# Kernel optimization log

Measured on AMD Instinct MI355X. Metric: run time of the kernel, lower is better.

## Reference

```python
import jax, jax.numpy as jnp
import numpy as np

HID_DIM = 1024
B, S = 8, 2048
SCALE = float(np.sqrt(HID_DIM))
NEG = -1e10


def setup_inputs() -> dict:
    key = jax.random.key(0)
    ks = jax.random.split(key, 13)
    d = HID_DIM
    std = 1.0 / np.sqrt(d)
    return {
        "query": jax.random.normal(ks[0], (B, S, d), jnp.float32),
        "key_": jax.random.normal(ks[1], (B, S, d), jnp.float32),
        "value": jax.random.normal(ks[2], (B, S, d), jnp.float32),
        "mask": jax.random.randint(ks[3], (B, S), 0, 2, jnp.int32),
        "Wq": jax.random.uniform(ks[4], (d, d), jnp.float32, -std, std),
        "bq": jax.random.uniform(ks[5], (d,), jnp.float32, -std, std),
        "Wk": jax.random.uniform(ks[6], (d, d), jnp.float32, -std, std),
        "bk": jax.random.uniform(ks[7], (d,), jnp.float32, -std, std),
        "Wv": jax.random.uniform(ks[8], (d, d), jnp.float32, -std, std),
        "bv": jax.random.uniform(ks[9], (d,), jnp.float32, -std, std),
        "Wfc": jax.random.uniform(ks[10], (d, d), jnp.float32, -std, std),
        "bfc": jax.random.uniform(ks[11], (d,), jnp.float32, -std, std),
    }


def reference(query, key_, value, mask, Wq, bq, Wk, bk, Wv, bv, Wfc, bfc):
    # Linear projections (torch Linear: x @ W.T + b)
    Q = jnp.einsum("bsd,ed->bse", query, Wq) + bq
    K = jnp.einsum("bsd,ed->bse", key_, Wk) + bk
    V = jnp.einsum("bsd,ed->bse", value, Wv) + bv
    # Scaled dot-product energy: [B, S, S]
    energy = jnp.einsum("bqd,bkd->bqk", Q, K) / SCALE
    # Faithful to source: mask broadcast over last dim masks QUERY rows
    energy = jnp.where(mask[:, :, None] == 0, NEG, energy)
    attention = jax.nn.softmax(energy, axis=-1)  # dropout=0 (eval)
    x = jnp.einsum("bqk,bkd->bqd", attention, V)
    out = jnp.einsum("bsd,ed->bse", x, Wfc) + bfc
    return out
```

## Files before the change

### kernel.cpp

```cpp
#include <hip/hip_runtime.h>
#include <hip/hip_bf16.h>


#define DEVINL __device__ __forceinline__

typedef __bf16 bf16x8 __attribute__((ext_vector_type(8)));
typedef float f32x4 __attribute__((ext_vector_type(4)));

static constexpr int Bb = 8;
static constexpr int S = 2048;
static constexpr int D = 1024;

DEVINL unsigned short f32_to_bf16(float f) {
  unsigned u = __float_as_uint(f);
  u = (u + 0x7FFFu + ((u >> 16) & 1u)) >> 16;
  return (unsigned short)u;
}
DEVINL float bflo(unsigned u) { return __uint_as_float(u << 16); }
DEVINL float bfhi(unsigned u) { return __uint_as_float(u & 0xFFFF0000u); }

DEVINL void gload16(const unsigned short* g, char* l) {
  __builtin_amdgcn_global_load_lds((__attribute__((address_space(1))) void*)g,
                                   (__attribute__((address_space(3))) void*)l,
                                   16, 0, 0);
}
DEVINL void gload16u(const unsigned short* g, unsigned short* l) {
  gload16(g, (char*)l);
}

#define BAR() __builtin_amdgcn_s_barrier()
#define LGK0() asm volatile("s_waitcnt lgkmcnt(0)" ::: "memory")

#define PH_OPEN() \
  BAR();          \
  LGK0();         \
  __builtin_amdgcn_s_setprio(1)
#define PH_CLOSE()               \
  __builtin_amdgcn_s_setprio(0); \
  BAR()

#define MFMA_QUAD(A_, B_, MO, NO)                                              \
  {                                                                            \
    _Pragma("unroll") for (int mi_ = 0; mi_ < 4; mi_++) {                      \
      _Pragma("unroll") for (int nj_ = 0; nj_ < 2; nj_++) {                    \
        acc[(MO) + mi_][(NO) + nj_] = __builtin_amdgcn_mfma_f32_16x16x32_bf16( \
            A_[mi_][0], B_[nj_][0], acc[(MO) + mi_][(NO) + nj_], 0, 0, 0);     \
        acc[(MO) + mi_][(NO) + nj_] = __builtin_amdgcn_mfma_f32_16x16x32_bf16( \
            A_[mi_][1], B_[nj_][1], acc[(MO) + mi_][(NO) + nj_], 0, 0, 0);     \
      }                                                                        \
    }                                                                          \
  }

__global__ __launch_bounds__(256) void conv_f32_bf16(const float* __restrict__ in,
                                                     unsigned short* __restrict__ out,
                                                     int n8) {
  int i = blockIdx.x * 256 + threadIdx.x;
  int stride = gridDim.x * 256;
  for (; i < n8; i += stride) {
    const float4* p = (const float4*)in + (size_t)i * 2;
    float4 a = p[0], b = p[1];
    uint4 o;
    o.x = (unsigned)f32_to_bf16(a.x) | ((unsigned)f32_to_bf16(a.y) << 16);
    o.y = (unsigned)f32_to_bf16(a.z) | ((unsigned)f32_to_bf16(a.w) << 16);
    o.z = (unsigned)f32_to_bf16(b.x) | ((unsigned)f32_to_bf16(b.y) << 16);
    o.w = (unsigned)f32_to_bf16(b.z) | ((unsigned)f32_to_bf16(b.w) << 16);
    ((uint4*)out)[i] = o;
  }
}

__global__ __launch_bounds__(256) void conv_k_wvec(const float* __restrict__ in,
                                                   const float* __restrict__ g32,
                                                   unsigned short* __restrict__ xkB,
                                                   float* __restrict__ w32) {
  const int row = blockIdx.x * 4 + (threadIdx.x >> 6);
  const int lane = threadIdx.x & 63;
  const float* src = in + (size_t)row * 1024 + lane * 16;
  unsigned short* dst = xkB + (size_t)row * 1024 + lane * 16;
  float s = 0.f;
  uint4 o[2];
  unsigned* po = (unsigned*)o;
#pragma unroll
  for (int c = 0; c < 4; c++) {
    float4 v = *(const float4*)(src + c * 4);
    float4 g = *(const float4*)(g32 + lane * 16 + c * 4);
    unsigned lo = (unsigned)f32_to_bf16(v.x) | ((unsigned)f32_to_bf16(v.y) << 16);
    unsigned hi = (unsigned)f32_to_bf16(v.z) | ((unsigned)f32_to_bf16(v.w) << 16);
    po[c * 2] = lo;
    po[c * 2 + 1] = hi;
    s += bflo(lo) * g.x + bfhi(lo) * g.y + bflo(hi) * g.z + bfhi(hi) * g.w;
  }
  *(uint4*)dst = o[0];
  *(uint4*)(dst + 8) = o[1];
#pragma unroll
  for (int off = 32; off >= 1; off >>= 1) s += __shfl_xor(s, off);
  if (lane == 0) w32[row] = s;
}

__global__ __launch_bounds__(256) void tconv(const float* __restrict__ in,
                                             unsigned short* __restrict__ out,
                                             int R, int C) {
  __shared__ unsigned short t[64][72];
  const int c0 = blockIdx.x * 64, r0 = blockIdx.y * 64, b = blockIdx.z;
  in += (size_t)b * R * C;
  out += (size_t)b * R * C;
  const int tr = threadIdx.x >> 4;
  const int tc = threadIdx.x & 15;
#pragma unroll
  for (int i = 0; i < 4; i++) {
    int row = tr + i * 16;
    float4 v = *(const float4*)(in + (size_t)(r0 + row) * C + c0 + tc * 4);
    t[tc * 4 + 0][row] = f32_to_bf16(v.x);
    t[tc * 4 + 1][row] = f32_to_bf16(v.y);
    t[tc * 4 + 2][row] = f32_to_bf16(v.z);
    t[tc * 4 + 3][row] = f32_to_bf16(v.w);
  }
  __syncthreads();
  const int c = threadIdx.x >> 2, rs = (threadIdx.x & 3) * 16;
  unsigned short tmp[16];
#pragma unroll
  for (int j = 0; j < 16; j++) tmp[j] = t[c][rs + j];
  *(uint4*)(out + (size_t)(c0 + c) * R + r0 + rs) = *(const uint4*)&tmp[0];
  *(uint4*)(out + (size_t)(c0 + c) * R + r0 + rs + 8) = *(const uint4*)&tmp[8];
}

__global__ __launch_bounds__(256) void cvec_kernel(const float* __restrict__ Wfc,
                                                   const float* __restrict__ bv,
                                                   const float* __restrict__ bfc,
                                                   float* __restrict__ cv) {
  const int f = blockIdx.x;
  const float* row = Wfc + (size_t)f * 1024;
  float s = 0.f;
  for (int e = threadIdx.x; e < 1024; e += 256) s += row[e] * bv[e];
#pragma unroll
  for (int off = 32; off >= 1; off >>= 1) s += __shfl_xor(s, off);
  __shared__ float red[4];
  const int wave = threadIdx.x >> 6, lane = threadIdx.x & 63;
  if (lane == 0) red[wave] = s;
  __syncthreads();
  if (threadIdx.x == 0) cv[f] = red[0] + red[1] + red[2] + red[3] + bfc[f];
}

__global__ __launch_bounds__(256) void gvec_kernel(const unsigned short* __restrict__ WkT,
                                                   const float* __restrict__ bq,
                                                   float* __restrict__ g32) {
  const int e = blockIdx.x;
  const unsigned short* row = WkT + (size_t)e * 1024;
  const int j0 = threadIdx.x * 4;
  uint2 v = *(const uint2*)(row + j0);
  float4 b4 = *(const float4*)(bq + j0);
  float s = bflo(v.x) * b4.x + bfhi(v.x) * b4.y + bflo(v.y) * b4.z + bfhi(v.y) * b4.w;
#pragma unroll
  for (int off = 32; off >= 1; off >>= 1) s += __shfl_xor(s, off);
  __shared__ float red[4];
  const int wave = threadIdx.x >> 6, lane = threadIdx.x & 63;
  if (lane == 0) red[wave] = s;
  __syncthreads();
  if (threadIdx.x == 0) g32[e] = (red[0] + red[1] + red[2] + red[3]) * (1.0f / 32.0f);
}

__global__ __launch_bounds__(256) void mask_scan(const int* __restrict__ msk,
                                                 int* __restrict__ qidx,
                                                 int* __restrict__ midx,
                                                 int* __restrict__ cnts) {
  __shared__ int offs[257];
  const int b = blockIdx.x;
  const int* mrow = msk + b * 2048;
  const int base = threadIdx.x * 8;
  int m[8], c = 0;
#pragma unroll
  for (int i = 0; i < 8; i++) {
    m[i] = mrow[base + i];
    c += m[i];
  }
  offs[threadIdx.x + 1] = c;
  __syncthreads();
  if (threadIdx.x == 0) {
    offs[0] = 0;
    for (int j = 1; j <= 256; j++) offs[j] += offs[j - 1];
    int tot = offs[256];
    cnts[b] = tot;
    cnts[8 + b] = (tot + 127) & ~127;
    cnts[16 + b] = (tot + 255) & ~255;
    cnts[24 + b] = 2048 - tot;
  }
  __syncthreads();
  int u = offs[threadIdx.x];
#pragma unroll
  for (int i = 0; i < 8; i++) {
    int idx = base + i;
    if (m[i])
      qidx[b * 2048 + (u++)] = idx;
    else
      midx[b * 2048 + (idx - u)] = idx;
  }
}

__global__ __launch_bounds__(128) void compact_q(const float* __restrict__ q,
                                                 const int* __restrict__ qidx,
                                                 const int* __restrict__ cnts,
                                                 unsigned short* __restrict__ xqC) {
  const int r = blockIdx.x;
  const int b = r >> 11, i = r & 2047;
  if (i >= cnts[16 + b]) return;
  unsigned short* dst = xqC + ((size_t)b * 2048 + i) * 1024;
  if (i < cnts[b]) {
    const float* src = q + ((size_t)b * 2048 + qidx[b * 2048 + i]) * 1024 + threadIdx.x * 8;
    float4 a = *(const float4*)src;
    float4 c = *(const float4*)(src + 4);
    uint4 o;
    o.x = (unsigned)f32_to_bf16(a.x) | ((unsigned)f32_to_bf16(a.y) << 16);
    o.y = (unsigned)f32_to_bf16(a.z) | ((unsigned)f32_to_bf16(a.w) << 16);
    o.z = (unsigned)f32_to_bf16(c.x) | ((unsigned)f32_to_bf16(c.y) << 16);
    o.w = (unsigned)f32_to_bf16(c.z) | ((unsigned)f32_to_bf16(c.w) << 16);
    ((uint4*)dst)[threadIdx.x] = o;
  } else {
    ((uint4*)dst)[threadIdx.x] = make_uint4(0, 0, 0, 0);
  }
}

__global__ __launch_bounds__(64) void colmean_kernel(const unsigned short* __restrict__ vpT,
                                                     const float* __restrict__ cv,
                                                     float* __restrict__ cm) {
  const int f = blockIdx.x, b = blockIdx.y;
  const unsigned short* base = vpT + (size_t)f * 16384 + b * 2048 + threadIdx.x * 32;
  float s = 0.f;
#pragma unroll
  for (int c = 0; c < 4; c++) {
    uint4 v = ((const uint4*)base)[c];
    unsigned u[4] = {v.x, v.y, v.z, v.w};
#pragma unroll
    for (int i = 0; i < 4; i++) s += bflo(u[i]) + bfhi(u[i]);
  }
#pragma unroll
  for (int off = 32; off >= 1; off >>= 1) s += __shfl_xor(s, off);
  if (threadIdx.x == 0) cm[b * 1024 + f] = s * (1.0f / 2048.0f) + cv[f];
}

__global__ __launch_bounds__(128) void fill_masked(const int* __restrict__ midx,
                                                   const int* __restrict__ cnts,
                                                   const float* __restrict__ cm,
                                                   float* __restrict__ out) {
  const int r = blockIdx.x;
  const int b = r >> 11, j = r & 2047;
  if (j >= cnts[24 + b]) return;
  const int qr = midx[b * 2048 + j];
  float* dst = out + ((size_t)b * 2048 + qr) * 1024 + threadIdx.x * 8;
  const float* src = cm + b * 1024 + threadIdx.x * 8;
  *(float4*)dst = *(const float4*)src;
  *(float4*)(dst + 4) = *(const float4*)(src + 4);
}

__global__ __launch_bounds__(256) void rowinv_kernel(const float* __restrict__ partialT,
                                                     float* __restrict__ rowinv) {
  const int r = blockIdx.x * 256 + threadIdx.x;
  float s = 0.f;
#pragma unroll
  for (int c = 0; c < 32; c++) s += partialT[(size_t)c * 16384 + r];
  rowinv[r] = 1.0f / s;
}

__global__ __launch_bounds__(256) void gemm128(const unsigned short* __restrict__ A,
                                               const unsigned short* __restrict__ Bt,
                                               unsigned short* __restrict__ C,
                                               int M, int N, int K,
                                               long long bsA, long long bsB, long long bsC) {
  const int tid = threadIdx.x;
  const int wave = tid >> 6;
  const int lane = tid & 63;
  const int wr = wave >> 1, wc = wave & 1;
  const int m0 = blockIdx.y * 128, n0 = blockIdx.x * 128;
  A += (size_t)blockIdx.z * bsA;
  Bt += (size_t)blockIdx.z * bsB;
  C += (size_t)blockIdx.z * bsC;

  __shared__ unsigned short lds[2][2][128 * 32];

  const int srow = wave * 16 + (lane >> 2);
  const int scol = (lane & 3) * 8;
  const unsigned short* gA = A + (size_t)(m0 + srow) * K + scol;
  const unsigned short* gB = Bt + (size_t)(n0 + srow) * K + scol;

  f32x4 acc[4][4];
#pragma unroll
  for (int i = 0; i < 4; i++)
#pragma unroll
    for (int j = 0; j < 4; j++) acc[i][j] = (f32x4){0.f, 0.f, 0.f, 0.f};

  const int nk = K >> 5;
  auto stage = [&](int buf, int kt) {
    const unsigned short* a0 = gA + (size_t)kt * 32;
    const unsigned short* b0 = gB + (size_t)kt * 32;
    unsigned short* la = &lds[buf][0][wave * 512];
    unsigned short* lb = &lds[buf][1][wave * 512];
    gload16u(a0, la);
    gload16u(a0 + (size_t)64 * K, la + 2048);
    gload16u(b0, lb);
    gload16u(b0 + (size_t)64 * K, lb + 2048);
  };

  stage(0, 0);
  asm volatile("s_waitcnt vmcnt(0)" ::: "memory");
  __syncthreads();

  const int fm = lane & 15;
  const int fk = (lane >> 4) * 8;

  int cur = 0;
  for (int t = 0; t < nk; ++t) {
    if (t + 1 < nk) stage(cur ^ 1, t + 1);
    bf16x8 af[4], bfr[4];
#pragma unroll
    for (int i = 0; i < 4; i++)
      af[i] = *(const bf16x8*)&lds[cur][0][(wr * 64 + i * 16 + fm) * 32 + fk];
#pragma unroll
    for (int j = 0; j < 4; j++)
      bfr[j] = *(const bf16x8*)&lds[cur][1][(wc * 64 + j * 16 + fm) * 32 + fk];
#pragma unroll
    for (int i = 0; i < 4; i++)
#pragma unroll
      for (int j = 0; j < 4; j++)
        acc[i][j] = __builtin_amdgcn_mfma_f32_16x16x32_bf16(af[i], bfr[j], acc[i][j], 0, 0, 0);
    asm volatile("s_waitcnt vmcnt(0)" ::: "memory");
    __syncthreads();
    cur ^= 1;
  }

  const int en = n0 + wc * 64 + fm;
  const int em = m0 + wr * 64 + ((lane >> 4) << 2);
#pragma unroll
  for (int j = 0; j < 4; j++)
#pragma unroll
    for (int i = 0; i < 4; i++)
#pragma unroll
      for (int r = 0; r < 4; r++)
        C[(size_t)(em + i * 16 + r) * N + en + j * 16] = f32_to_bf16(acc[i][j][r]);
}

template <int OUTMODE>
__global__ __launch_bounds__(256, 3) void gemm128c(
    const unsigned short* __restrict__ A, const unsigned short* __restrict__ Bt,
    const float* __restrict__ aux,
    const float* __restrict__ bias,
    const int* __restrict__ cnts, const int* __restrict__ qidx,
    float* __restrict__ partialT, void* __restrict__ Cv,
    int N, int K, int lda, int ldb,
    long long bsA, long long bsB, long long bsC, float scale) {
  __shared__ unsigned short lds[2][2][128 * 32];
  char* smem = (char*)&lds[0][0][0];
  const int tid = threadIdx.x;
  const int wave = tid >> 6, lane = tid & 63;
  const int wm = wave >> 1, wn = wave & 1;

  const int gx = gridDim.x, gy = gridDim.y;
  const int nwg = gx * gy * (int)gridDim.z;
  const int wg = blockIdx.x + gx * (blockIdx.y + gy * blockIdx.z);
  const int swz = (wg & 7) * (nwg >> 3) + (wg >> 3);
  const int bx = swz % gx;
  const int rem = swz / gx;
  const int by = rem % gy;
  const int bz = rem / gy;

  const int m0 = by * 128, n0 = bx * 128;
  if (OUTMODE == 3) {
    if (n0 >= cnts[8 + bz]) return;
  } else {
    if (m0 >= cnts[8 + bz]) return;
  }
  A += (size_t)bz * bsA;
  Bt += (size_t)bz * bsB;

  const int srow = wave * 16 + (lane >> 2);
  const int scol = (lane & 3) * 8;
  const unsigned short* gA = A + (size_t)(m0 + srow) * lda + scol;
  const unsigned short* gB = Bt + (size_t)(n0 + srow) * ldb + scol;

  f32x4 acc[4][4];
#pragma unroll
  for (int i = 0; i < 4; i++)
#pragma unroll
    for (int j = 0; j < 4; j++) acc[i][j] = (f32x4){0.f, 0.f, 0.f, 0.f};

  const int nk = K >> 5;
  auto stage = [&](int buf, int kt) {
    const unsigned short* a0 = gA + (size_t)kt * 32;
    const unsigned short* b0 = gB + (size_t)kt * 32;
    unsigned short* la = &lds[buf][0][wave * 512];
    unsigned short* lb = &lds[buf][1][wave * 512];
    gload16u(a0, la);
    gload16u(a0 + (size_t)64 * lda, la + 2048);
    gload16u(b0, lb);
    gload16u(b0 + (size_t)64 * ldb, lb + 2048);
  };

  stage(0, 0);
  asm volatile("s_waitcnt vmcnt(0)" ::: "memory");
  __syncthreads();

  const int fm = lane & 15;
  const int fk = (lane >> 4) * 8;

  int cur = 0;
  for (int t = 0; t < nk; ++t) {
    if (t + 1 < nk) stage(cur ^ 1, t + 1);
    bf16x8 af[4], bfr[4];
#pragma unroll
    for (int i = 0; i < 4; i++)
      af[i] = *(const bf16x8*)&lds[cur][0][(wm * 64 + i * 16 + fm) * 32 + fk];
#pragma unroll
    for (int j = 0; j < 4; j++)
      bfr[j] = *(const bf16x8*)&lds[cur][1][(wn * 64 + j * 16 + fm) * 32 + fk];
    __builtin_amdgcn_s_setprio(1);
#pragma unroll
    for (int i = 0; i < 4; i++)
#pragma unroll
      for (int j = 0; j < 4; j++)
        acc[i][j] = __builtin_amdgcn_mfma_f32_16x16x32_bf16(af[i], bfr[j], acc[i][j], 0, 0, 0);
    __builtin_amdgcn_s_setprio(0);
    asm volatile("s_waitcnt vmcnt(0)" ::: "memory");
    __syncthreads();
    cur ^= 1;
  }

  const int fr = lane & 15;
  const int fg = lane >> 4;

  if (OUTMODE == 3) {
    const int keyrow0 = m0 + wm * 64 + fg * 4;
    const int colq = wn * 64 + fr;
    float psum[4] = {0.f, 0.f, 0.f, 0.f};
#pragma unroll
    for (int mi = 0; mi < 4; mi++) {
      const float4 w4 = *(const float4*)&aux[bz * 2048 + keyrow0 + mi * 16];
      const int lrow = wm * 64 + fg * 4 + mi * 16;
#pragma unroll
      for (int nj = 0; nj < 4; nj++) {
        float p0 = __expf(fmaf(acc[mi][nj][0], scale, w4.x));
        float p1 = __expf(fmaf(acc[mi][nj][1], scale, w4.y));
        float p2 = __expf(fmaf(acc[mi][nj][2], scale, w4.z));
        float p3 = __expf(fmaf(acc[mi][nj][3], scale, w4.w));
        psum[nj] += (p0 + p1) + (p2 + p3);
        unsigned lo = (unsigned)f32_to_bf16(p0) | ((unsigned)f32_to_bf16(p1) << 16);
        unsigned hi = (unsigned)f32_to_bf16(p2) | ((unsigned)f32_to_bf16(p3) << 16);
        const int c = colq + nj * 16;
        const int byte = c * 256 + ((((lrow >> 3) ^ (c & 7)) << 4) | ((lrow & 4) << 1));
        *(uint2*)(smem + byte) = make_uint2(lo, hi);
      }
    }
#pragma unroll
    for (int nj = 0; nj < 4; nj++) {
      psum[nj] += __shfl_xor(psum[nj], 16);
      psum[nj] += __shfl_xor(psum[nj], 32);
    }
    if (fg == 0) {
#pragma unroll
      for (int nj = 0; nj < 4; nj++)
        partialT[(size_t)(by * 2 + wm) * 16384 + bz * 2048 + n0 + colq + nj * 16] = psum[nj];
    }
    __syncthreads();
    unsigned short* Eb = (unsigned short*)Cv + (size_t)bz * bsC;
    const int qh = wave * 2 + (lane >> 5);
    const int kq = (lane & 31) * 4;
#pragma unroll
    for (int p = 0; p < 16; p++) {
      const int ql = qh + p * 8;
      const int byte = ql * 256 + ((((kq >> 3) ^ (ql & 7)) << 4) | ((kq & 4) << 1));
      uint2 vv = *(const uint2*)(smem + byte);
      *(uint2*)(Eb + (size_t)(n0 + ql) * 2048 + m0 + kq) = vv;
    }
  } else {
    float* C = (float*)Cv + (size_t)bz * bsC;
    const int* qx = qidx + bz * 2048;
    const int cb = cnts[bz];
    const int row0base = m0 + wm * 64 + fg * 4;
    const int colbase = n0 + wn * 64 + fr;
#pragma unroll
    for (int mi = 0; mi < 4; mi++) {
      const int j0 = row0base + mi * 16;
      const float4 ri = *(const float4*)&aux[bz * 2048 + j0];
      int qr[4];
      bool ok[4];
#pragma unroll
      for (int r = 0; r < 4; r++) {
        ok[r] = (j0 + r) < cb;
        qr[r] = ok[r] ? qx[j0 + r] : 0;
      }
#pragma unroll
      for (int nj = 0; nj < 4; nj++) {
        const int col = colbase + nj * 16;
        const float cvv = bias[col];
        if (ok[0]) C[(size_t)qr[0] * N + col] = fmaf(acc[mi][nj][0], ri.x, cvv);
        if (ok[1]) C[(size_t)qr[1] * N + col] = fmaf(acc[mi][nj][1], ri.y, cvv);
        if (ok[2]) C[(size_t)qr[2] * N + col] = fmaf(acc[mi][nj][2], ri.z, cvv);
        if (ok[3]) C[(size_t)qr[3] * N + col] = fmaf(acc[mi][nj][3], ri.w, cvv);
      }
    }
  }
}

template <int OUTMODE, bool HAS_BIAS, int EXITMODE>
__global__ __launch_bounds__(512, 2) void gemm256(
    const unsigned short* __restrict__ A, const unsigned short* __restrict__ Bt,
    const float* __restrict__ bias, const int* __restrict__ cnts,
    const int* __restrict__ qidx, float* __restrict__ partial,
    void* __restrict__ Cv, int M, int N, int K, int lda, int ldb,
    long long bsA, long long bsB, long long bsC, float scale) {
  extern __shared__ char smem[];
  const int tid = threadIdx.x;
  const int wave = tid >> 6, lane = tid & 63;
  const int wr = wave >> 2, wc = wave & 3;

  const int gx = gridDim.x, gy = gridDim.y;
  const int nwg = gx * gy * (int)gridDim.z;
  const int wg = blockIdx.x + gx * (blockIdx.y + gy * blockIdx.z);
  const int swz = (wg & 7) * (nwg >> 3) + (wg >> 3);
  const int bx = swz % gx;
  const int rem = swz / gx;
  const int by = rem % gy;
  const int bz = rem / gy;

  const int m0 = by * 256, n0 = bx * 256;
  if (EXITMODE == 1) {
    if ((n0 & 2047) >= cnts[16 + (n0 >> 11)]) return;
  }
  A += (size_t)bz * bsA;
  Bt += (size_t)bz * bsB;

  const int rl = lane >> 3;
  const int gl = (lane & 7) ^ rl;
  const unsigned short* gA = A + (size_t)(m0 + wave * 8 + rl) * lda + gl * 8;
  const unsigned short* gB = Bt + (size_t)(n0 + wave * 8 + rl) * ldb + gl * 8;

  auto stageA = [&](int db, int t, int h) {
    const unsigned short* g = gA + (size_t)(h * 128) * lda + (size_t)t * 64;
    char* l = smem + db * 65536 + h * 16384 + wave * 1024;
    gload16(g, l);
    gload16(g + (size_t)64 * lda, l + 8192);
  };
  auto stageB = [&](int db, int t, int h) {
    const unsigned short* g = gB + (size_t)(h * 128) * ldb + (size_t)t * 64;
    char* l = smem + db * 65536 + 32768 + h * 16384 + wave * 1024;
    gload16(g, l);
    gload16(g + (size_t)64 * ldb, l + 8192);
  };

  const int fr = lane & 15;
  const int fg = lane >> 4;
  auto readA = [&](int db, int mi, int kc) -> bf16x8 {
    const int row = wr * 128 + mi * 16 + fr;
    const int g = (kc * 4 + fg) ^ (row & 7);
    return *(const bf16x8*)(smem + db * 65536 + row * 128 + g * 16);
  };
  auto readB = [&](int db, int nj, int kc) -> bf16x8 {
    const int row = wc * 64 + nj * 16 + fr;
    const int g = (kc * 4 + fg) ^ (row & 7);
    return *(const bf16x8*)(smem + db * 65536 + 32768 + row * 128 + g * 16);
  };

  f32x4 acc[8][4];
#pragma unroll
  for (int i = 0; i < 8; i++)
#pragma unroll
    for (int j = 0; j < 4; j++) acc[i][j] = (f32x4){0.f, 0.f, 0.f, 0.f};

  stageA(0, 0, 0);
  stageA(0, 0, 1);
  stageB(0, 0, 0);
  stageB(0, 0, 1);
  stageB(1, 1, 0);
  stageB(1, 1, 1);
  asm volatile("s_waitcnt vmcnt(4)" ::: "memory");
  BAR();

  const int nt = K >> 6;
  const int niter = nt >> 1;

  for (int j = 0; j < niter; ++j) {
    const int t0 = 2 * j, t1 = 2 * j + 1;
    const bool more = (j + 1 < niter);
    bf16x8 a[4][2], b0[2][2], b1[2][2];

#pragma unroll
    for (int mi = 0; mi < 4; mi++) { a[mi][0] = readA(0, mi, 0); a[mi][1] = readA(0, mi, 1); }
#pragma unroll
    for (int nj = 0; nj < 2; nj++) { b0[nj][0] = readB(0, nj, 0); b0[nj][1] = readB(0, nj, 1); }
    stageA(1, t1, 0);
    asm volatile("s_waitcnt lgkmcnt(8)" ::: "memory");
    PH_OPEN();
    MFMA_QUAD(a, b0, 0, 0);
    PH_CLOSE();

#pragma unroll
    for (int nj = 0; nj < 2; nj++) { b1[nj][0] = readB(0, nj + 2, 0); b1[nj][1] = readB(0, nj + 2, 1); }
    stageA(1, t1, 1);
    PH_OPEN();
    MFMA_QUAD(a, b1, 0, 2);
    PH_CLOSE();

#pragma unroll
    for (int mi = 0; mi < 4; mi++) { a[mi][0] = readA(0, mi + 4, 0); a[mi][1] = readA(0, mi + 4, 1); }
    if (more) stageB(0, t0 + 2, 0);
    PH_OPEN();
    MFMA_QUAD(a, b0, 4, 0);
    PH_CLOSE();

    if (more) stageB(0, t0 + 2, 1);
    BAR();
    __builtin_amdgcn_s_setprio(1);
    MFMA_QUAD(a, b1, 4, 2);
    __builtin_amdgcn_s_setprio(0);
    if (more)
      asm volatile("s_waitcnt vmcnt(4)" ::: "memory");
    else
      asm volatile("s_waitcnt vmcnt(0)" ::: "memory");
    BAR();

#pragma unroll
    for (int mi = 0; mi < 4; mi++) { a[mi][0] = readA(1, mi, 0); a[mi][1] = readA(1, mi, 1); }
#pragma unroll
    for (int nj = 0; nj < 2; nj++) { b0[nj][0] = readB(1, nj, 0); b0[nj][1] = readB(1, nj, 1); }
    if (more) stageA(0, t0 + 2, 0);
    asm volatile("s_waitcnt lgkmcnt(8)" ::: "memory");
    PH_OPEN();
    MFMA_QUAD(a, b0, 0, 0);
    PH_CLOSE();

#pragma unroll
    for (int nj = 0; nj < 2; nj++) { b1[nj][0] = readB(1, nj + 2, 0); b1[nj][1] = readB(1, nj + 2, 1); }
    if (more) stageA(0, t0 + 2, 1);
    PH_OPEN();
    MFMA_QUAD(a, b1, 0, 2);
    PH_CLOSE();

#pragma unroll
    for (int mi = 0; mi < 4; mi++) { a[mi][0] = readA(1, mi + 4, 0); a[mi][1] = readA(1, mi + 4, 1); }
    if (more) stageB(1, t1 + 2, 0);
    PH_OPEN();
    MFMA_QUAD(a, b0, 4, 0);
    PH_CLOSE();

    if (more) stageB(1, t1 + 2, 1);
    BAR();
    __builtin_amdgcn_s_setprio(1);
    MFMA_QUAD(a, b1, 4, 2);
    __builtin_amdgcn_s_setprio(0);
    asm volatile("s_waitcnt vmcnt(4)" ::: "memory");
    BAR();
  }

  const int row0base = m0 + wr * 128 + fg * 4;

  {
    const int lcol = wc * 64 + fr;
    const int lrow0 = wr * 128 + fg * 4;
#pragma unroll
    for (int mi = 0; mi < 8; mi++) {
      const int lrow = lrow0 + mi * 16;
      float4 bw = make_float4(0.f, 0.f, 0.f, 0.f);
      if (HAS_BIAS) bw = *(const float4*)&bias[row0base + mi * 16];
#pragma unroll
      for (int nj = 0; nj < 4; nj++) {
        float v0 = acc[mi][nj][0] + bw.x;
        float v1 = acc[mi][nj][1] + bw.y;
        float v2 = acc[mi][nj][2] + bw.z;
        float v3 = acc[mi][nj][3] + bw.w;
        unsigned lo = (unsigned)f32_to_bf16(v0) | ((unsigned)f32_to_bf16(v1) << 16);
        unsigned hi = (unsigned)f32_to_bf16(v2) | ((unsigned)f32_to_bf16(v3) << 16);
        const int c = lcol + nj * 16;
        const int byte = c * 512 + ((((lrow >> 3) ^ (c & 7)) << 4) | ((lrow & 4) << 1));
        *(uint2*)(smem + byte) = make_uint2(lo, hi);
      }
    }
    __syncthreads();
    unsigned short* C = (unsigned short*)Cv + (size_t)bz * bsC;
    const int qh = wave * 2 + (lane >> 5);
    const int kl = (lane & 31) * 8;
#pragma unroll
    for (int p = 0; p < 16; p++) {
      const int ql = qh + p * 16;
      const int byte = ql * 512 + ((((kl >> 3) ^ (ql & 7)) << 4));
      uint4 vv = *(const uint4*)(smem + byte);
      *(uint4*)(C + (size_t)(n0 + ql) * M + m0 + kl) = vv;
    }
  }
}

extern "C" void kernel_launch(void* const* d_in, const int* in_sizes, int n_in,
                              void* d_out, int out_size, void* d_ws, size_t ws_size,
                              hipStream_t stream) {
  const float* q = (const float*)d_in[0];
  const float* k_ = (const float*)d_in[1];
  const float* v = (const float*)d_in[2];
  const int* msk = (const int*)d_in[3];
  const float* Wq = (const float*)d_in[4];
  const float* bq = (const float*)d_in[5];
  const float* Wk = (const float*)d_in[6];
  const float* Wv = (const float*)d_in[8];
  const float* bv = (const float*)d_in[9];
  const float* Wfc = (const float*)d_in[10];
  const float* bfc = (const float*)d_in[11];

  char* ws = (char*)d_ws;
  const size_t MB = 1u << 20;
  const size_t KB = 1u << 10;
  unsigned short* WkT = (unsigned short*)(ws + 0 * MB);
  unsigned short* WfcB = (unsigned short*)(ws + 2 * MB);
  unsigned short* WqT = (unsigned short*)(ws + 4 * MB);
  unsigned short* WvT = (unsigned short*)(ws + 6 * MB);
  unsigned short* Mt = (unsigned short*)(ws + 8 * MB);
  unsigned short* W2 = (unsigned short*)(ws + 10 * MB);
  float* partialT = (float*)(ws + 12 * MB);
  float* rowinv = (float*)(ws + 14 * MB);
  float* cv = (float*)(ws + 14 * MB + 64 * KB);
  float* g32 = (float*)(ws + 14 * MB + 128 * KB);
  float* w32 = (float*)(ws + 14 * MB + 192 * KB);
  int* qidx = (int*)(ws + 14 * MB + 256 * KB);
  int* midx = (int*)(ws + 14 * MB + 320 * KB);
  int* cnts = (int*)(ws + 14 * MB + 384 * KB);
  float* cm = (float*)(ws + 14 * MB + 512 * KB);
  unsigned short* Qc = (unsigned short*)(ws + 16 * MB);
  unsigned short* xkB = (unsigned short*)(ws + 48 * MB);
  unsigned short* vpT = (unsigned short*)(ws + 80 * MB);
  unsigned short* xqC = (unsigned short*)(ws + 112 * MB);
  unsigned short* vB = (unsigned short*)(ws + 144 * MB);
  unsigned short* E = (unsigned short*)(ws + 112 * MB);

  const int NBS = Bb * S * D;

  auto conv = [&](const float* in, unsigned short* out, int n) {
    int n8 = n / 8;
    int blocks = (n8 + 255) / 256;
    if (blocks > 2048) blocks = 2048;
    conv_f32_bf16<<<dim3(blocks), dim3(256), 0, stream>>>(in, out, n8);
  };

  tconv<<<dim3(16, 16, 1), dim3(256), 0, stream>>>(Wq, WqT, D, D);
  tconv<<<dim3(16, 16, 1), dim3(256), 0, stream>>>(Wk, WkT, D, D);
  conv(Wfc, WfcB, D * D);
  tconv<<<dim3(16, 16, 1), dim3(256), 0, stream>>>(Wv, WvT, D, D);
  gemm128<<<dim3(8, 8, 2), dim3(256), 0, stream>>>(
      WkT, WqT, Mt, D, D, D, (long long)D * D, (long long)D * D, (long long)D * D);
  cvec_kernel<<<dim3(1024), dim3(256), 0, stream>>>(Wfc, bv, bfc, cv);
  gvec_kernel<<<dim3(1024), dim3(256), 0, stream>>>(WkT, bq, g32);

  mask_scan<<<dim3(8), dim3(256), 0, stream>>>(msk, qidx, midx, cnts);
  compact_q<<<dim3(16384), dim3(128), 0, stream>>>(q, qidx, cnts, xqC);

  const float invscale = 1.0f / 32.0f;

  gemm256<1, false, 1><<<dim3(64, 4, 1), dim3(512), 131072, stream>>>(
      Mt, xqC, nullptr, cnts, nullptr, nullptr, Qc, D, Bb * S, D, D, D,
      0, 0, 0, 1.0f);
  conv_k_wvec<<<dim3(4096), dim3(256), 0, stream>>>(k_, g32, xkB, w32);
  conv(v, vB, NBS);
  gemm256<1, false, 0><<<dim3(4, 64, 1), dim3(512), 131072, stream>>>(
      vB, W2, nullptr, nullptr, nullptr, nullptr, vpT, Bb * S, D, D, D, D,
      0, 0, 0, 1.0f);
  colmean_kernel<<<dim3(1024, 8), dim3(64), 0, stream>>>(vpT, cv, cm);
  gemm128c<3><<<dim3(16, 16, 8), dim3(256), 0, stream>>>(
      xkB, Qc, w32, nullptr, cnts, nullptr, partialT, E,
      D, 1024, 1024, 1024, (long long)S * D, (long long)S * D,
      (long long)S * S, invscale);
  rowinv_kernel<<<dim3(64), dim3(256), 0, stream>>>(partialT, rowinv);
  gemm128c<6><<<dim3(8, 16, 8), dim3(256), 0, stream>>>(
      E, vpT, rowinv, cv, cnts, qidx, nullptr, d_out,
      D, 2048, 2048, Bb * S, (long long)S * S, (long long)S,
      (long long)S * D, 1.0f);
  fill_masked<<<dim3(16384), dim3(128), 0, stream>>>(midx, cnts, cm, (float*)d_out);
}
```

Baseline: 297.5 us.

## Reassociate value projection after attention so W2 GEMM runs on compacted rows

Instead of projecting all value rows through W2 before attention, the attention-weighted sum is computed on transposed raw values and the W2 projection is applied afterward on the compacted query rows only. Column means for masked rows are computed from raw value means followed by a small matrix-vector product. This removes the full-size value projection GEMM over all rows, at the cost of an extra intermediate bf16 buffer and an additional GEMM launch.

```diff
diff --git a/kernel.cpp b/kernel.cpp
--- a/kernel.cpp
+++ b/kernel.cpp
@@ -218,11 +218,10 @@
   }
 }
 
-__global__ __launch_bounds__(64) void colmean_kernel(const unsigned short* __restrict__ vpT,
-                                                     const float* __restrict__ cv,
-                                                     float* __restrict__ cm) {
-  const int f = blockIdx.x, b = blockIdx.y;
-  const unsigned short* base = vpT + (size_t)f * 16384 + b * 2048 + threadIdx.x * 32;
+__global__ __launch_bounds__(64) void colmean_v(const unsigned short* __restrict__ vT,
+                                                float* __restrict__ cmv) {
+  const int e = blockIdx.x, b = blockIdx.y;
+  const unsigned short* base = vT + (size_t)b * 2097152 + (size_t)e * 2048 + threadIdx.x * 32;
   float s = 0.f;
 #pragma unroll
   for (int c = 0; c < 4; c++) {
@@ -233,7 +232,26 @@
   }
 #pragma unroll
   for (int off = 32; off >= 1; off >>= 1) s += __shfl_xor(s, off);
-  if (threadIdx.x == 0) cm[b * 1024 + f] = s * (1.0f / 2048.0f) + cv[f];
+  if (threadIdx.x == 0) cmv[b * 1024 + e] = s * (1.0f / 2048.0f);
+}
+
+__global__ __launch_bounds__(256) void cmw_kernel(const float* __restrict__ cmv,
+                                                  const unsigned short* __restrict__ W2,
+                                                  const float* __restrict__ cv,
+                                                  float* __restrict__ cm) {
+  const int f = blockIdx.x, b = blockIdx.y;
+  const unsigned short* row = W2 + (size_t)f * 1024;
+  const int j0 = threadIdx.x * 4;
+  uint2 v = *(const uint2*)(row + j0);
+  float4 c4 = *(const float4*)(cmv + b * 1024 + j0);
+  float s = bflo(v.x) * c4.x + bfhi(v.x) * c4.y + bflo(v.y) * c4.z + bfhi(v.y) * c4.w;
+#pragma unroll
+  for (int off = 32; off >= 1; off >>= 1) s += __shfl_xor(s, off);
+  __shared__ float red[4];
+  const int wave = threadIdx.x >> 6, lane = threadIdx.x & 63;
+  if (lane == 0) red[wave] = s;
+  __syncthreads();
+  if (threadIdx.x == 0) cm[b * 1024 + f] = red[0] + red[1] + red[2] + red[3] + cv[f];
 }
 
 __global__ __launch_bounds__(128) void fill_masked(const int* __restrict__ midx,
@@ -361,7 +379,7 @@
   const int bz = rem / gy;
 
   const int m0 = by * 128, n0 = bx * 128;
-  if (OUTMODE == 3) {
+  if (OUTMODE == 3 || OUTMODE == 4) {
     if (n0 >= cnts[8 + bz]) return;
   } else {
     if (m0 >= cnts[8 + bz]) return;
@@ -465,7 +483,39 @@
       const int ql = qh + p * 8;
       const int byte = ql * 256 + ((((kq >> 3) ^ (ql & 7)) << 4) | ((kq & 4) << 1));
       uint2 vv = *(const uint2*)(smem + byte);
-      *(uint2*)(Eb + (size_t)(n0 + ql) * 2048 + m0 + kq) = vv;
+      *(uint2*)(Eb + (size_t)(n0 + ql) * N + m0 + kq) = vv;
+    }
+  } else if (OUTMODE == 4) {
+    const int colq = wn * 64 + fr;
+    float ri[4];
+#pragma unroll
+    for (int nj = 0; nj < 4; nj++) ri[nj] = aux[bz * 2048 + n0 + colq + nj * 16];
+#pragma unroll
+    for (int mi = 0; mi < 4; mi++) {
+      const int lrow = wm * 64 + fg * 4 + mi * 16;
+#pragma unroll
+      for (int nj = 0; nj < 4; nj++) {
+        float v0 = acc[mi][nj][0] * ri[nj];
+        float v1 = acc[mi][nj][1] * ri[nj];
+        float v2 = acc[mi][nj][2] * ri[nj];
+        float v3 = acc[mi][nj][3] * ri[nj];
+        unsigned lo = (unsigned)f32_to_bf16(v0) | ((unsigned)f32_to_bf16(v1) << 16);
+        unsigned hi = (unsigned)f32_to_bf16(v2) | ((unsigned)f32_to_bf16(v3) << 16);
+        const int c = colq + nj * 16;
+        const int byte = c * 256 + ((((lrow >> 3) ^ (c & 7)) << 4) | ((lrow & 4) << 1));
+        *(uint2*)(smem + byte) = make_uint2(lo, hi);
+      }
+    }
+    __syncthreads();
+    unsigned short* Cb = (unsigned short*)Cv + (size_t)bz * bsC;
+    const int qh = wave * 2 + (lane >> 5);
+    const int kq = (lane & 31) * 4;
+#pragma unroll
+    for (int p = 0; p < 16; p++) {
+      const int ql = qh + p * 8;
+      const int byte = ql * 256 + ((((kq >> 3) ^ (ql & 7)) << 4) | ((kq & 4) << 1));
+      uint2 vv = *(const uint2*)(smem + byte);
+      *(uint2*)(Cb + (size_t)(n0 + ql) * N + m0 + kq) = vv;
     }
   } else {
     float* C = (float*)Cv + (size_t)bz * bsC;
@@ -476,7 +526,8 @@
 #pragma unroll
     for (int mi = 0; mi < 4; mi++) {
       const int j0 = row0base + mi * 16;
-      const float4 ri = *(const float4*)&aux[bz * 2048 + j0];
+      float4 ri = make_float4(1.f, 1.f, 1.f, 1.f);
+      if (aux) ri = *(const float4*)&aux[bz * 2048 + j0];
       int qr[4];
       bool ok[4];
 #pragma unroll
@@ -717,14 +768,13 @@
   int* midx = (int*)(ws + 14 * MB + 320 * KB);
   int* cnts = (int*)(ws + 14 * MB + 384 * KB);
   float* cm = (float*)(ws + 14 * MB + 512 * KB);
+  float* cmv = (float*)(ws + 14 * MB + 576 * KB);
   unsigned short* Qc = (unsigned short*)(ws + 16 * MB);
   unsigned short* xkB = (unsigned short*)(ws + 48 * MB);
-  unsigned short* vpT = (unsigned short*)(ws + 80 * MB);
+  unsigned short* valueT = (unsigned short*)(ws + 80 * MB);
   unsigned short* xqC = (unsigned short*)(ws + 112 * MB);
-  unsigned short* vB = (unsigned short*)(ws + 144 * MB);
-  unsigned short* E = (unsigned short*)(ws + 112 * MB);
-
-  const int NBS = Bb * S * D;
+  unsigned short* E = (unsigned short*)(ws + 144 * MB);
+  unsigned short* y = Qc;
 
   auto conv = [&](const float* in, unsigned short* out, int n) {
     int n8 = n / 8;
@@ -751,19 +801,21 @@
       Mt, xqC, nullptr, cnts, nullptr, nullptr, Qc, D, Bb * S, D, D, D,
       0, 0, 0, 1.0f);
   conv_k_wvec<<<dim3(4096), dim3(256), 0, stream>>>(k_, g32, xkB, w32);
-  conv(v, vB, NBS);
-  gemm256<1, false, 0><<<dim3(4, 64, 1), dim3(512), 131072, stream>>>(
-      vB, W2, nullptr, nullptr, nullptr, nullptr, vpT, Bb * S, D, D, D, D,
-      0, 0, 0, 1.0f);
-  colmean_kernel<<<dim3(1024, 8), dim3(64), 0, stream>>>(vpT, cv, cm);
+  tconv<<<dim3(16, 32, 8), dim3(256), 0, stream>>>(v, valueT, S, D);
+  colmean_v<<<dim3(1024, 8), dim3(64), 0, stream>>>(valueT, cmv);
+  cmw_kernel<<<dim3(1024, 8), dim3(256), 0, stream>>>(cmv, W2, cv, cm);
   gemm128c<3><<<dim3(16, 16, 8), dim3(256), 0, stream>>>(
       xkB, Qc, w32, nullptr, cnts, nullptr, partialT, E,
-      D, 1024, 1024, 1024, (long long)S * D, (long long)S * D,
+      2048, 1024, 1024, 1024, (long long)S * D, (long long)S * D,
       (long long)S * S, invscale);
   rowinv_kernel<<<dim3(64), dim3(256), 0, stream>>>(partialT, rowinv);
+  gemm128c<4><<<dim3(16, 8, 8), dim3(256), 0, stream>>>(
+      valueT, E, rowinv, nullptr, cnts, nullptr, nullptr, y,
+      1024, 2048, 2048, 2048, (long long)D * S, (long long)S * S,
+      (long long)S * D, 1.0f);
   gemm128c<6><<<dim3(8, 16, 8), dim3(256), 0, stream>>>(
-      E, vpT, rowinv, cv, cnts, qidx, nullptr, d_out,
-      D, 2048, 2048, Bb * S, (long long)S * S, (long long)S,
+      y, W2, nullptr, cv, cnts, qidx, nullptr, d_out,
+      1024, 1024, 1024, 1024, (long long)S * D, 0,
       (long long)S * D, 1.0f);
   fill_masked<<<dim3(16384), dim3(128), 0, stream>>>(midx, cnts, cm, (float*)d_out);
 }
```

Result: slower. 311.5 us (+4.7%).
